# Kernel tuning notes

Hardware: AMD Instinct MI355X
Metric: run time of the kernel (lower is better)

The kernel has to match this reference:

```python
import jax, jax.numpy as jnp
import numpy as np

L, H, NH, FF = 12, 768, 12, 3072
HD = H // NH
B, T = 8, 512
SCALE = 1.0 / float(np.sqrt(HD))
EPS = 1e-12


def setup_inputs() -> dict:
    key = jax.random.key(0)
    ks = jax.random.split(key, 10)
    s = jnp.float32(0.02)

    def p(k, shape):
        return jax.random.normal(k, shape, dtype=jnp.float32) * s

    return {
        "hidden_states": jax.random.normal(ks[0], (B, T, H), dtype=jnp.float32),
        "attention_mask": jnp.ones((B, T), dtype=jnp.float32),
        "Wq": p(ks[1], (L, H, H)), "bq": jnp.zeros((L, H), jnp.float32),
        "Wk": p(ks[2], (L, H, H)), "bk": jnp.zeros((L, H), jnp.float32),
        "Wv": p(ks[3], (L, H, H)), "bv": jnp.zeros((L, H), jnp.float32),
        "Wao": p(ks[4], (L, H, H)), "bao": jnp.zeros((L, H), jnp.float32),
        "ln1_g": jnp.ones((L, H), jnp.float32), "ln1_b": jnp.zeros((L, H), jnp.float32),
        "Wi": p(ks[5], (L, H, FF)), "bi": jnp.zeros((L, FF), jnp.float32),
        "Wo": p(ks[6], (L, FF, H)), "bo": jnp.zeros((L, H), jnp.float32),
        "ln2_g": jnp.ones((L, H), jnp.float32), "ln2_b": jnp.zeros((L, H), jnp.float32),
    }


def _layernorm(x, g, b):
    m = jnp.mean(x, axis=-1, keepdims=True)
    v = jnp.mean((x - m) ** 2, axis=-1, keepdims=True)
    return (x - m) * jax.lax.rsqrt(v + EPS) * g + b


def _encoder(hidden_states, attention_mask, params):
    # additive mask: (1 - mask) * -10000, broadcast to [B, 1, 1, T]
    add_mask = (1.0 - attention_mask)[:, None, None, :] * -10000.0

    def layer(x, p):
        wq, bq, wk, bk, wv, bv, wao, bao, g1, b1, wi, bi, wo, bo, g2, b2 = p
        q = (x @ wq + bq).reshape(B, T, NH, HD)
        k = (x @ wk + bk).reshape(B, T, NH, HD)
        v = (x @ wv + bv).reshape(B, T, NH, HD)
        scores = jnp.einsum('bihd,bjhd->bhij', q, k) * SCALE + add_mask
        probs = jax.nn.softmax(scores, axis=-1)  # dropout p=0 (eval)
        ctx = jnp.einsum('bhij,bjhd->bihd', probs, v).reshape(B, T, H)
        attn_out = _layernorm(ctx @ wao + bao + x, g1, b1)
        ff = jax.nn.gelu(attn_out @ wi + bi, approximate=False)
        out = _layernorm(ff @ wo + bo + attn_out, g2, b2)
        return out, None

    out, _ = jax.lax.scan(layer, hidden_states, params)
    return out


def reference(hidden_states, attention_mask, Wq, bq, Wk, bk, Wv, bv, Wao, bao,
              ln1_g, ln1_b, Wi, bi, Wo, bo, ln2_g, ln2_b):
    params = (Wq, bq, Wk, bk, Wv, bv, Wao, bao, ln1_g, ln1_b, Wi, bi, Wo, bo, ln2_g, ln2_b)
    return _encoder(hidden_states, attention_mask, params)
```

## Files before the change

kernel.cpp:

```cpp
#include <hip/hip_runtime.h>
#include <hip/hip_bf16.h>

typedef __bf16 bf16;
typedef __attribute__((ext_vector_type(8))) __bf16 bf16x8;
typedef __attribute__((ext_vector_type(4))) float f32x4;

#define MFMA16(a, b, c) __builtin_amdgcn_mfma_f32_16x16x32_bf16((a), (b), (c), 0, 0, 0)

__device__ __forceinline__ void async16(const bf16* g, bf16* l) {
    __builtin_amdgcn_global_load_lds((__attribute__((address_space(1))) void*)(g),
                                     (__attribute__((address_space(3))) void*)(l), 16, 0, 0);
}

template <int MODE>
__global__ __launch_bounds__(256) void gemm_kernel(
    const bf16* __restrict__ A, const bf16* __restrict__ WT,
    const float* __restrict__ b0, const float* __restrict__ b1, const float* __restrict__ b2,
    int s1, int s2,
    void* __restrict__ o0, void* __restrict__ o1, void* __restrict__ o2,
    int M, int N, int K, int Kpart)
{
    __shared__ __align__(16) bf16 sA[2][128 * 32];
    __shared__ __align__(16) bf16 sB[2][128 * 32];

    const int tid  = threadIdx.x;
    const int lane = tid & 63;
    const int wave = tid >> 6;
    const int quad = lane >> 4;
    const int l15  = lane & 15;
    const int wm   = (wave >> 1) * 64;
    const int wn   = (wave & 1) * 64;
    const int bm   = blockIdx.y * 128;
    const int bn   = blockIdx.x * 128;
    const int kbase = blockIdx.z * Kpart;

    f32x4 acc[4][4];
#pragma unroll
    for (int i = 0; i < 4; i++)
#pragma unroll
        for (int j = 0; j < 4; j++)
#pragma unroll
            for (int r = 0; r < 4; r++) acc[i][j][r] = 0.0f;

    const int idx0 = tid;
    const int idx1 = tid + 256;
    const int ra0 = idx0 >> 2, ca0 = (idx0 & 3) * 8;
    const int ra1 = idx1 >> 2, ca1 = (idx1 & 3) * 8;

    const bf16* Arow0 = A  + (size_t)(bm + ra0) * K + kbase + ca0;
    const bf16* Arow1 = A  + (size_t)(bm + ra1) * K + kbase + ca1;
    const bf16* Brow0 = WT + (size_t)(bn + ra0) * K + kbase + ca0;
    const bf16* Brow1 = WT + (size_t)(bn + ra1) * K + kbase + ca1;

    const int nk = Kpart >> 5;

    async16(Arow0, sA[0] + idx0 * 8);
    async16(Arow1, sA[0] + idx1 * 8);
    async16(Brow0, sB[0] + idx0 * 8);
    async16(Brow1, sB[0] + idx1 * 8);
    __syncthreads();

    int cur = 0;
    for (int kt = 0; kt < nk; kt++) {
        if (kt + 1 < nk) {
            const int ko = (kt + 1) * 32;
            async16(Arow0 + ko, sA[cur ^ 1] + idx0 * 8);
            async16(Arow1 + ko, sA[cur ^ 1] + idx1 * 8);
            async16(Brow0 + ko, sB[cur ^ 1] + idx0 * 8);
            async16(Brow1 + ko, sB[cur ^ 1] + idx1 * 8);
        }
        bf16x8 af[4], bfr[4];
#pragma unroll
        for (int i = 0; i < 4; i++)
            af[i] = *(const bf16x8*)(sA[cur] + (wm + i * 16 + l15) * 32 + quad * 8);
#pragma unroll
        for (int i = 0; i < 4; i++)
            bfr[i] = *(const bf16x8*)(sB[cur] + (wn + i * 16 + l15) * 32 + quad * 8);
#pragma unroll
        for (int mt = 0; mt < 4; mt++)
#pragma unroll
            for (int nt = 0; nt < 4; nt++)
                acc[mt][nt] = MFMA16(af[mt], bfr[nt], acc[mt][nt]);
        __syncthreads();
        cur ^= 1;
    }

    void* outp = (blockIdx.z == 0) ? o0 : (blockIdx.z == 1) ? o1 : o2;

#pragma unroll
    for (int nt = 0; nt < 4; nt++) {
        const int col = bn + wn + nt * 16 + l15;
        float bias = 0.0f;
        if (MODE != 1)
            bias = (col < s1) ? b0[col] : (col < s2) ? b1[col - s1] : b2[col - s2];
#pragma unroll
        for (int mt = 0; mt < 4; mt++) {
#pragma unroll
            for (int r = 0; r < 4; r++) {
                const int row = bm + wm + mt * 16 + quad * 4 + r;
                float v = acc[mt][nt][r] + bias;
                if (MODE == 2) v = 0.5f * v * (1.0f + erff(v * 0.70710678118654752f));
                if (MODE == 1) ((float*)outp)[(size_t)row * N + col] = v;
                else           ((bf16*)outp)[(size_t)row * N + col] = (bf16)v;
            }
        }
    }
}

__global__ __launch_bounds__(256) void vtrans_kernel(
    const bf16* __restrict__ qkv, bf16* __restrict__ vT)
{
    const int bh = blockIdx.y;
    const int b = bh / 12, h = bh - b * 12;
    const int k0 = blockIdx.x * 128;
    __shared__ __align__(16) bf16 tile[128 * 72];
    const int tid = threadIdx.x;
    const bf16* src = qkv + (size_t)(b * 512 + k0) * 2304 + 1536 + h * 64;
#pragma unroll
    for (int i = 0; i < 4; i++) {
        const int idx = i * 256 + tid;
        const int r = idx >> 3, c = (idx & 7) * 8;
        *(uint4*)(tile + r * 72 + c) = *(const uint4*)(src + (size_t)r * 2304 + c);
    }
    __syncthreads();
    bf16* dst = vT + (size_t)bh * 64 * 512 + k0;
#pragma unroll
    for (int i = 0; i < 4; i++) {
        const int idx = i * 256 + tid;
        const int d = idx & 63, kg = idx >> 6;
        alignas(16) bf16 tmp[8];
#pragma unroll
        for (int e = 0; e < 8; e++) tmp[e] = tile[(kg * 8 + e) * 72 + d];
        *(uint4*)(dst + (size_t)d * 512 + kg * 8) = *(uint4*)tmp;
    }
}

__global__ __launch_bounds__(256) void attn_kernel(
    const bf16* __restrict__ qkv, const bf16* __restrict__ vT,
    const float* __restrict__ mask, bf16* __restrict__ ctx)
{
    const int b = blockIdx.z, h = blockIdx.y, q0 = blockIdx.x * 32;
    const int bh = b * 12 + h;
    const int tid = threadIdx.x, lane = tid & 63, wave = tid >> 6;
    const int quad = lane >> 4, l15 = lane & 15;
    const int mt = wave & 1;
    const int whi = wave >> 1;

    __shared__ __align__(16) bf16 sQ[32 * 80];
    __shared__ __align__(16) bf16 sKV[64 * 80];
    __shared__ __align__(16) bf16 sS[32 * 520];
    __shared__ float sAM[512];
    __shared__ float sRedM[32 * 8];
    __shared__ float sRedS[32 * 8];
    __shared__ float sRow[32];

    for (int i = tid; i < 512; i += 256)
        sAM[i] = (1.0f - mask[b * 512 + i]) * -10000.0f;

    const size_t RS = 2304;
    {
        const int r = tid >> 3, c = (tid & 7) * 8;
        *(uint4*)(sQ + r * 80 + c) =
            *(const uint4*)(qkv + (size_t)(b * 512 + q0 + r) * RS + h * 64 + c);
    }

#pragma unroll 1
    for (int kt = 0; kt < 8; kt++) {
        __syncthreads();
        const bf16* Kb = qkv + (size_t)(b * 512 + kt * 64) * RS + 768 + h * 64;
#pragma unroll
        for (int i = 0; i < 2; i++) {
            const int idx = i * 256 + tid;
            const int r = idx >> 3, c = (idx & 7) * 8;
            *(uint4*)(sKV + r * 80 + c) = *(const uint4*)(Kb + (size_t)r * RS + c);
        }
        __syncthreads();
        bf16x8 aQ0 = *(const bf16x8*)(sQ + (mt * 16 + l15) * 80 + quad * 8);
        bf16x8 aQ1 = *(const bf16x8*)(sQ + (mt * 16 + l15) * 80 + 32 + quad * 8);
#pragma unroll
        for (int n = 0; n < 2; n++) {
            const int nt = whi * 2 + n;
            f32x4 accS;
#pragma unroll
            for (int r = 0; r < 4; r++) accS[r] = 0.0f;
            accS = MFMA16(aQ0, *(const bf16x8*)(sKV + (nt * 16 + l15) * 80 + quad * 8), accS);
            accS = MFMA16(aQ1, *(const bf16x8*)(sKV + (nt * 16 + l15) * 80 + 32 + quad * 8), accS);
#pragma unroll
            for (int r = 0; r < 4; r++) {
                const int row = mt * 16 + quad * 4 + r;
                sS[row * 520 + kt * 64 + nt * 16 + l15] = (bf16)accS[r];
            }
        }
    }
    __syncthreads();

    {
        const int r = tid >> 3, p = tid & 7;
        float mx = -1e30f;
#pragma unroll
        for (int t = 0; t < 8; t++) {
            const int v0 = (p + 8 * t) * 8;
            bf16x8 pv = *(const bf16x8*)(sS + r * 520 + v0);
#pragma unroll
            for (int e = 0; e < 8; e++)
                mx = fmaxf(mx, (float)pv[e] * 0.125f + sAM[v0 + e]);
        }
        sRedM[r * 8 + p] = mx;
        __syncthreads();
#pragma unroll
        for (int q = 0; q < 8; q++) mx = fmaxf(mx, sRedM[r * 8 + q]);
        float sum = 0.0f;
#pragma unroll
        for (int t = 0; t < 8; t++) {
            const int v0 = (p + 8 * t) * 8;
            bf16x8 pv = *(const bf16x8*)(sS + r * 520 + v0);
            bf16x8 ev;
#pragma unroll
            for (int e = 0; e < 8; e++) {
                const float x = __expf((float)pv[e] * 0.125f + sAM[v0 + e] - mx);
                sum += x;
                ev[e] = (bf16)x;
            }
            *(bf16x8*)(sS + r * 520 + v0) = ev;
        }
        sRedS[r * 8 + p] = sum;
        __syncthreads();
        if (p == 0) {
            float s = 0.0f;
#pragma unroll
            for (int q = 0; q < 8; q++) s += sRedS[r * 8 + q];
            sRow[r] = s;
        }
    }

    f32x4 accO[2];
#pragma unroll
    for (int i = 0; i < 2; i++)
#pragma unroll
        for (int r = 0; r < 4; r++) accO[i][r] = 0.0f;

#pragma unroll 1
    for (int kt = 0; kt < 8; kt++) {
        __syncthreads();
        const bf16* Vt = vT + (size_t)bh * 64 * 512 + kt * 64;
#pragma unroll
        for (int i = 0; i < 2; i++) {
            const int idx = i * 256 + tid;
            const int r = idx >> 3, c = (idx & 7) * 8;
            *(uint4*)(sKV + r * 80 + c) = *(const uint4*)(Vt + (size_t)r * 512 + c);
        }
        __syncthreads();
#pragma unroll
        for (int kk = 0; kk < 2; kk++) {
            bf16x8 aP = *(const bf16x8*)(sS + (mt * 16 + l15) * 520 + kt * 64 + kk * 32 + quad * 8);
#pragma unroll
            for (int n = 0; n < 2; n++) {
                bf16x8 bV = *(const bf16x8*)(sKV + (whi * 32 + n * 16 + l15) * 80 + kk * 32 + quad * 8);
                accO[n] = MFMA16(aP, bV, accO[n]);
            }
        }
    }
#pragma unroll
    for (int n = 0; n < 2; n++) {
#pragma unroll
        for (int r = 0; r < 4; r++) {
            const int row = mt * 16 + quad * 4 + r;
            const float o = accO[n][r] / sRow[row];
            ctx[(size_t)(b * 512 + q0 + row) * 768 + h * 64 + whi * 32 + n * 16 + l15] = (bf16)o;
        }
    }
}

template <int NP>
__global__ __launch_bounds__(256) void ln_kernel(
    const float* __restrict__ p0, const float* __restrict__ p1, const float* __restrict__ p2,
    const float* __restrict__ bias, const float* __restrict__ resid,
    const float* __restrict__ g, const float* __restrict__ bb,
    bf16* __restrict__ out_bf, float* __restrict__ out_f32)
{
    const int row = blockIdx.x;
    const int tid = threadIdx.x;
    __shared__ float sS[4], sQ[4];

    float x[3], s = 0.0f, sq = 0.0f;
#pragma unroll
    for (int j = 0; j < 3; j++) {
        const int c = tid + j * 256;
        const size_t idx = (size_t)row * 768 + c;
        float v = p0[idx] + bias[c] + resid[idx];
        if (NP > 1) v += p1[idx];
        if (NP > 2) v += p2[idx];
        x[j] = v; s += v; sq += v * v;
    }
#pragma unroll
    for (int off = 32; off; off >>= 1) { s += __shfl_down(s, off); sq += __shfl_down(sq, off); }
    if ((tid & 63) == 0) { sS[tid >> 6] = s; sQ[tid >> 6] = sq; }
    __syncthreads();
    s  = sS[0] + sS[1] + sS[2] + sS[3];
    sq = sQ[0] + sQ[1] + sQ[2] + sQ[3];
    const float mean = s * (1.0f / 768.0f);
    float var = sq * (1.0f / 768.0f) - mean * mean;
    var = fmaxf(var, 0.0f);
    const float rstd = rsqrtf(var + 1e-12f);
#pragma unroll
    for (int j = 0; j < 3; j++) {
        const int c = tid + j * 256;
        const float v = (x[j] - mean) * rstd * g[c] + bb[c];
        out_bf[(size_t)row * 768 + c] = (bf16)v;
        out_f32[(size_t)row * 768 + c] = v;
    }
}

__global__ __launch_bounds__(256) void transpose_kernel(
    const float* __restrict__ Wq, const float* __restrict__ Wk, const float* __restrict__ Wv,
    const float* __restrict__ Wao, const float* __restrict__ Wi, const float* __restrict__ Wo,
    bf16* __restrict__ wT)
{
    __shared__ bf16 tile[64 * 68];
    int id = blockIdx.x;
    const float* src; bf16* dst; int Kd, Nd;
    if (id < 576) {
        const int w = id / 144; id -= w * 144;
        Kd = 768; Nd = 768;
        src = (w == 0) ? Wq : (w == 1) ? Wk : (w == 2) ? Wv : Wao;
        dst = wT + (size_t)w * 589824;
    } else if (id < 1152) {
        id -= 576; Kd = 768; Nd = 3072; src = Wi; dst = wT + 2359296;
    } else {
        id -= 1152; Kd = 3072; Nd = 768; src = Wo; dst = wT + 4718592;
    }
    const int tn = Nd >> 6;
    const int tr = id / tn, tc = id - tr * tn;
    const int r0 = tr * 64, c0 = tc * 64;
    const int tid = threadIdx.x;

#pragma unroll
    for (int i = 0; i < 4; i++) {
        const int idx = i * 256 + tid;
        const int r = idx >> 4, c4 = (idx & 15) * 4;
        const float4 f = *(const float4*)(src + (size_t)(r0 + r) * Nd + c0 + c4);
        alignas(8) bf16 q[4] = {(bf16)f.x, (bf16)f.y, (bf16)f.z, (bf16)f.w};
        *(ushort4*)(tile + r * 68 + c4) = *(ushort4*)q;
    }
    __syncthreads();
#pragma unroll
    for (int i = 0; i < 4; i++) {
        const int idx = i * 256 + tid;
        const int n = idx >> 4, kc = (idx & 15) * 4;
        alignas(8) bf16 tmp[4];
#pragma unroll
        for (int e = 0; e < 4; e++) tmp[e] = tile[(kc + e) * 68 + n];
        *(ushort4*)(dst + (size_t)(c0 + n) * Kd + r0 + kc) = *(ushort4*)tmp;
    }
}

__global__ __launch_bounds__(256) void convert_kernel(
    const float* __restrict__ in, bf16* __restrict__ out, int n)
{
    const int i = blockIdx.x * 256 + threadIdx.x;
    if (i < n) out[i] = (bf16)in[i];
}

extern "C" void kernel_launch(void* const* d_in, const int* in_sizes, int n_in,
                              void* d_out, int out_size, void* d_ws, size_t ws_size,
                              hipStream_t stream)
{
    const float* hidden = (const float*)d_in[0];
    const float* mask   = (const float*)d_in[1];
    const float* Wq  = (const float*)d_in[2];  const float* bq  = (const float*)d_in[3];
    const float* Wk  = (const float*)d_in[4];  const float* bk  = (const float*)d_in[5];
    const float* Wv  = (const float*)d_in[6];  const float* bv  = (const float*)d_in[7];
    const float* Wao = (const float*)d_in[8];  const float* bao = (const float*)d_in[9];
    const float* g1  = (const float*)d_in[10]; const float* be1 = (const float*)d_in[11];
    const float* Wi  = (const float*)d_in[12]; const float* bi  = (const float*)d_in[13];
    const float* Wo  = (const float*)d_in[14]; const float* bo  = (const float*)d_in[15];
    const float* g2  = (const float*)d_in[16]; const float* be2 = (const float*)d_in[17];

    char* ws = (char*)d_ws;
    bf16*  wT    = (bf16*)(ws);
    bf16*  qkv   = (bf16*)(ws + 14155776);
    bf16*  vT    = (bf16*)(ws + 33030144);
    bf16*  ctx   = (bf16*)(ws + 39321600);
    bf16*  attnb = (bf16*)(ws + 45613056);
    bf16*  xb    = (bf16*)(ws + 51904512);
    float* xf    = (float*)(ws + 58195968);
    float* attnf = (float*)(ws + 70778880);
    bf16*  ffh   = (bf16*)(ws + 14155776);
    float* pA0   = (float*)(ws + 14155776);
    float* pA1   = (float*)(ws + 26738688);
    float* pF0   = (float*)(ws + 39321600);
    float* pF1   = (float*)(ws + 83361792);
    float* pF2   = (float*)d_out;

    convert_kernel<<<12288, 256, 0, stream>>>(hidden, xb, 3145728);

    for (int l = 0; l < 12; l++) {
        transpose_kernel<<<1728, 256, 0, stream>>>(
            Wq + (size_t)l * 589824, Wk + (size_t)l * 589824, Wv + (size_t)l * 589824,
            Wao + (size_t)l * 589824, Wi + (size_t)l * 2359296, Wo + (size_t)l * 2359296, wT);

        gemm_kernel<0><<<dim3(18, 32, 1), 256, 0, stream>>>(
            xb, wT, bq + l * 768, bk + l * 768, bv + l * 768, 768, 1536,
            qkv, nullptr, nullptr, 4096, 2304, 768, 768);

        vtrans_kernel<<<dim3(4, 96), 256, 0, stream>>>(qkv, vT);

        attn_kernel<<<dim3(16, 12, 8), 256, 0, stream>>>(qkv, vT, mask, ctx);

        gemm_kernel<1><<<dim3(6, 32, 2), 256, 0, stream>>>(
            ctx, wT + 1769472, nullptr, nullptr, nullptr, 0, 0,
            pA0, pA1, nullptr, 4096, 768, 768, 384);

        const float* resid1 = (l == 0) ? hidden : xf;
        ln_kernel<2><<<4096, 256, 0, stream>>>(
            pA0, pA1, nullptr, bao + l * 768, resid1, g1 + l * 768, be1 + l * 768, attnb, attnf);

        gemm_kernel<2><<<dim3(24, 32, 1), 256, 0, stream>>>(
            attnb, wT + 2359296, bi + l * 3072, bi + l * 3072, bi + l * 3072, 3072, 3072,
            ffh, nullptr, nullptr, 4096, 3072, 768, 768);

        gemm_kernel<1><<<dim3(6, 32, 3), 256, 0, stream>>>(
            ffh, wT + 4718592, nullptr, nullptr, nullptr, 0, 0,
            pF0, pF1, pF2, 4096, 768, 3072, 1024);

        float* f32dst = (l == 11) ? (float*)d_out : xf;
        ln_kernel<3><<<4096, 256, 0, stream>>>(
            pF0, pF1, pF2, bo + l * 768, attnf, g2 + l * 768, be2 + l * 768, xb, f32dst);
    }
}
```

Baseline: 2.507 ms.

## Add BM=64 GEMM tiles, XCD-aware block swizzle, and fewer split-K partials

Templates the GEMM on block-M so the QKV, attention-output and FFN-down GEMMs use 64-row tiles with more blocks instead of split-K. The FFN-down split drops from three partials to two and the attention-output split-K is removed, so the layernorm kernels read fewer fp32 partial buffers. An XCD swizzle remaps block indices so that consecutive tiles land on the same XCD, which should improve L2 reuse for the GEMMs and attention. Smaller tiles lower per-block arithmetic intensity and raise the ratio of shared-memory loads to MFMAs.

```diff
diff --git a/kernel.cpp b/kernel.cpp
--- a/kernel.cpp
+++ b/kernel.cpp
@@ -12,15 +12,29 @@
                                      (__attribute__((address_space(3))) void*)(l), 16, 0, 0);
 }
 
-template <int MODE>
+__device__ __forceinline__ void xcd_swizzle(int& bx, int& by, int& bz) {
+    const int gx = gridDim.x, gy = gridDim.y;
+    const int nwg = gx * gy * gridDim.z;
+    const int lin = blockIdx.x + gx * (blockIdx.y + gy * blockIdx.z);
+    const int xcd = lin & 7, seq = lin >> 3;
+    const int q = nwg >> 3, r = nwg & 7;
+    const int nl = (xcd < r ? xcd * (q + 1) : r * (q + 1) + (xcd - r) * q) + seq;
+    bx = nl % gx;
+    const int t = nl / gx;
+    by = t % gy;
+    bz = t / gy;
+}
+
+template <int MODE, int BM>
 __global__ __launch_bounds__(256) void gemm_kernel(
     const bf16* __restrict__ A, const bf16* __restrict__ WT,
     const float* __restrict__ b0, const float* __restrict__ b1, const float* __restrict__ b2,
     int s1, int s2,
-    void* __restrict__ o0, void* __restrict__ o1, void* __restrict__ o2,
-    int M, int N, int K, int Kpart)
-{
-    __shared__ __align__(16) bf16 sA[2][128 * 32];
+    void* __restrict__ o0, void* __restrict__ o1,
+    int N, int K, int Kpart)
+{
+    constexpr int MT = BM / 32;
+    __shared__ __align__(16) bf16 sA[2][BM * 32];
     __shared__ __align__(16) bf16 sB[2][128 * 32];
 
     const int tid  = threadIdx.x;
@@ -28,35 +42,37 @@
     const int wave = tid >> 6;
     const int quad = lane >> 4;
     const int l15  = lane & 15;
-    const int wm   = (wave >> 1) * 64;
+    const int wm   = (wave >> 1) * (BM / 2);
     const int wn   = (wave & 1) * 64;
-    const int bm   = blockIdx.y * 128;
-    const int bn   = blockIdx.x * 128;
-    const int kbase = blockIdx.z * Kpart;
-
-    f32x4 acc[4][4];
-#pragma unroll
-    for (int i = 0; i < 4; i++)
+
+    int bxs, bys, bzs;
+    xcd_swizzle(bxs, bys, bzs);
+    const int bm = bys * BM;
+    const int bn = bxs * 128;
+    const int kbase = bzs * Kpart;
+
+    f32x4 acc[MT][4];
+#pragma unroll
+    for (int i = 0; i < MT; i++)
 #pragma unroll
         for (int j = 0; j < 4; j++)
 #pragma unroll
             for (int r = 0; r < 4; r++) acc[i][j][r] = 0.0f;
 
-    const int idx0 = tid;
     const int idx1 = tid + 256;
-    const int ra0 = idx0 >> 2, ca0 = (idx0 & 3) * 8;
-    const int ra1 = idx1 >> 2, ca1 = (idx1 & 3) * 8;
+    const int ra0 = tid  >> 2, ca0 = (tid  & 3) * 8;
+    const int rb1 = idx1 >> 2, cb1 = (idx1 & 3) * 8;
 
     const bf16* Arow0 = A  + (size_t)(bm + ra0) * K + kbase + ca0;
-    const bf16* Arow1 = A  + (size_t)(bm + ra1) * K + kbase + ca1;
+    const bf16* Arow1 = A  + (size_t)(bm + rb1) * K + kbase + cb1;
     const bf16* Brow0 = WT + (size_t)(bn + ra0) * K + kbase + ca0;
-    const bf16* Brow1 = WT + (size_t)(bn + ra1) * K + kbase + ca1;
+    const bf16* Brow1 = WT + (size_t)(bn + rb1) * K + kbase + cb1;
 
     const int nk = Kpart >> 5;
 
-    async16(Arow0, sA[0] + idx0 * 8);
-    async16(Arow1, sA[0] + idx1 * 8);
-    async16(Brow0, sB[0] + idx0 * 8);
+    async16(Arow0, sA[0] + tid * 8);
+    if (BM == 128) async16(Arow1, sA[0] + idx1 * 8);
+    async16(Brow0, sB[0] + tid * 8);
     async16(Brow1, sB[0] + idx1 * 8);
     __syncthreads();
 
@@ -64,20 +80,20 @@
     for (int kt = 0; kt < nk; kt++) {
         if (kt + 1 < nk) {
             const int ko = (kt + 1) * 32;
-            async16(Arow0 + ko, sA[cur ^ 1] + idx0 * 8);
-            async16(Arow1 + ko, sA[cur ^ 1] + idx1 * 8);
-            async16(Brow0 + ko, sB[cur ^ 1] + idx0 * 8);
+            async16(Arow0 + ko, sA[cur ^ 1] + tid * 8);
+            if (BM == 128) async16(Arow1 + ko, sA[cur ^ 1] + idx1 * 8);
+            async16(Brow0 + ko, sB[cur ^ 1] + tid * 8);
             async16(Brow1 + ko, sB[cur ^ 1] + idx1 * 8);
         }
-        bf16x8 af[4], bfr[4];
-#pragma unroll
-        for (int i = 0; i < 4; i++)
+        bf16x8 af[MT], bfr[4];
+#pragma unroll
+        for (int i = 0; i < MT; i++)
             af[i] = *(const bf16x8*)(sA[cur] + (wm + i * 16 + l15) * 32 + quad * 8);
 #pragma unroll
         for (int i = 0; i < 4; i++)
             bfr[i] = *(const bf16x8*)(sB[cur] + (wn + i * 16 + l15) * 32 + quad * 8);
 #pragma unroll
-        for (int mt = 0; mt < 4; mt++)
+        for (int mt = 0; mt < MT; mt++)
 #pragma unroll
             for (int nt = 0; nt < 4; nt++)
                 acc[mt][nt] = MFMA16(af[mt], bfr[nt], acc[mt][nt]);
@@ -85,7 +101,7 @@
         cur ^= 1;
     }
 
-    void* outp = (blockIdx.z == 0) ? o0 : (blockIdx.z == 1) ? o1 : o2;
+    void* outp = (bzs == 0) ? o0 : o1;
 
 #pragma unroll
     for (int nt = 0; nt < 4; nt++) {
@@ -94,7 +110,7 @@
         if (MODE != 1)
             bias = (col < s1) ? b0[col] : (col < s2) ? b1[col - s1] : b2[col - s2];
 #pragma unroll
-        for (int mt = 0; mt < 4; mt++) {
+        for (int mt = 0; mt < MT; mt++) {
 #pragma unroll
             for (int r = 0; r < 4; r++) {
                 const int row = bm + wm + mt * 16 + quad * 4 + r;
@@ -139,7 +155,9 @@
     const bf16* __restrict__ qkv, const bf16* __restrict__ vT,
     const float* __restrict__ mask, bf16* __restrict__ ctx)
 {
-    const int b = blockIdx.z, h = blockIdx.y, q0 = blockIdx.x * 32;
+    int bxs, bys, bzs;
+    xcd_swizzle(bxs, bys, bzs);
+    const int b = bzs, h = bys, q0 = bxs * 32;
     const int bh = b * 12 + h;
     const int tid = threadIdx.x, lane = tid & 63, wave = tid >> 6;
     const int quad = lane >> 4, l15 = lane & 15;
@@ -273,7 +291,7 @@
 
 template <int NP>
 __global__ __launch_bounds__(256) void ln_kernel(
-    const float* __restrict__ p0, const float* __restrict__ p1, const float* __restrict__ p2,
+    const float* __restrict__ p0, const float* __restrict__ p1,
     const float* __restrict__ bias, const float* __restrict__ resid,
     const float* __restrict__ g, const float* __restrict__ bb,
     bf16* __restrict__ out_bf, float* __restrict__ out_f32)
@@ -289,7 +307,6 @@
         const size_t idx = (size_t)row * 768 + c;
         float v = p0[idx] + bias[c] + resid[idx];
         if (NP > 1) v += p1[idx];
-        if (NP > 2) v += p2[idx];
         x[j] = v; s += v; sq += v * v;
     }
 #pragma unroll
@@ -387,10 +404,8 @@
     float* attnf = (float*)(ws + 70778880);
     bf16*  ffh   = (bf16*)(ws + 14155776);
     float* pA0   = (float*)(ws + 14155776);
-    float* pA1   = (float*)(ws + 26738688);
     float* pF0   = (float*)(ws + 39321600);
     float* pF1   = (float*)(ws + 83361792);
-    float* pF2   = (float*)d_out;
 
     convert_kernel<<<12288, 256, 0, stream>>>(hidden, xb, 3145728);
 
@@ -399,32 +414,32 @@
             Wq + (size_t)l * 589824, Wk + (size_t)l * 589824, Wv + (size_t)l * 589824,
             Wao + (size_t)l * 589824, Wi + (size_t)l * 2359296, Wo + (size_t)l * 2359296, wT);
 
-        gemm_kernel<0><<<dim3(18, 32, 1), 256, 0, stream>>>(
+        gemm_kernel<0, 64><<<dim3(18, 64, 1), 256, 0, stream>>>(
             xb, wT, bq + l * 768, bk + l * 768, bv + l * 768, 768, 1536,
-            qkv, nullptr, nullptr, 4096, 2304, 768, 768);
+            qkv, nullptr, 2304, 768, 768);
 
         vtrans_kernel<<<dim3(4, 96), 256, 0, stream>>>(qkv, vT);
 
         attn_kernel<<<dim3(16, 12, 8), 256, 0, stream>>>(qkv, vT, mask, ctx);
 
-        gemm_kernel<1><<<dim3(6, 32, 2), 256, 0, stream>>>(
+        gemm_kernel<1, 64><<<dim3(6, 64, 1), 256, 0, stream>>>(
             ctx, wT + 1769472, nullptr, nullptr, nullptr, 0, 0,
-            pA0, pA1, nullptr, 4096, 768, 768, 384);
+            pA0, nullptr, 768, 768, 768);
 
         const float* resid1 = (l == 0) ? hidden : xf;
+        ln_kernel<1><<<4096, 256, 0, stream>>>(
+            pA0, nullptr, bao + l * 768, resid1, g1 + l * 768, be1 + l * 768, attnb, attnf);
+
+        gemm_kernel<2, 128><<<dim3(24, 32, 1), 256, 0, stream>>>(
+            attnb, wT + 2359296, bi + l * 3072, bi + l * 3072, bi + l * 3072, 3072, 3072,
+            ffh, nullptr, 3072, 768, 768);
+
+        gemm_kernel<1, 64><<<dim3(6, 64, 2), 256, 0, stream>>>(
+            ffh, wT + 4718592, nullptr, nullptr, nullptr, 0, 0,
+            pF0, pF1, 768, 3072, 1536);
+
+        float* f32dst = (l == 11) ? (float*)d_out : xf;
         ln_kernel<2><<<4096, 256, 0, stream>>>(
-            pA0, pA1, nullptr, bao + l * 768, resid1, g1 + l * 768, be1 + l * 768, attnb, attnf);
-
-        gemm_kernel<2><<<dim3(24, 32, 1), 256, 0, stream>>>(
-            attnb, wT + 2359296, bi + l * 3072, bi + l * 3072, bi + l * 3072, 3072, 3072,
-            ffh, nullptr, nullptr, 4096, 3072, 768, 768);
-
-        gemm_kernel<1><<<dim3(6, 32, 3), 256, 0, stream>>>(
-            ffh, wT + 4718592, nullptr, nullptr, nullptr, 0, 0,
-            pF0, pF1, pF2, 4096, 768, 3072, 1024);
-
-        float* f32dst = (l == 11) ? (float*)d_out : xf;
-        ln_kernel<3><<<4096, 256, 0, stream>>>(
-            pF0, pF1, pF2, bo + l * 768, attnf, g2 + l * 768, be2 + l * 768, xb, f32dst);
-    }
-}
+            pF0, pF1, bo + l * 768, attnf, g2 + l * 768, be2 + l * 768, xb, f32dst);
+    }
+}
```

After: 2.513 ms. No clear change (+0.2%).
